# Performance work log

Measured on AMD Instinct MI355X. Metric: run time of the kernel, lower is better.

## Reference

```python
import jax, jax.numpy as jnp
import numpy as np

B, S, D, H, HD, F = 8, 1024, 512, 8, 64, 2048
EPS = 1e-6

def rmsnorm(x, w):
    var = jnp.mean(x * x, axis=-1, keepdims=True)
    return w * (x * jax.lax.rsqrt(var + EPS))

def setup_inputs() -> dict:
    key = jax.random.key(0)
    ks = jax.random.split(key, 10)
    sd = 512 ** -0.5
    return {
        "primals_1": jax.random.normal(ks[0], (D, D), jnp.float32) * sd,
        "primals_2": jax.random.normal(ks[1], (D, D), jnp.float32) * sd,
        "primals_3": jax.random.normal(ks[2], (D, D), jnp.float32) * sd,
        "primals_4": jax.random.normal(ks[3], (D, D), jnp.float32) * sd,
        "primals_5": jax.random.uniform(ks[4], (D,), jnp.float32, 0.5, 1.5),
        "primals_6": jax.random.normal(ks[5], (F, D), jnp.float32) * sd,
        "primals_7": jax.random.normal(ks[6], (D, F), jnp.float32) * (F ** -0.5),
        "primals_8": jax.random.uniform(ks[7], (D,), jnp.float32, 0.5, 1.5),
        "primals_9": jax.random.normal(ks[8], (B, S, D), jnp.float32),
        "primals_10": jax.random.normal(ks[9], (B, H, S, S), jnp.float32) * 0.1,
    }

def reference(primals_1, primals_2, primals_3, primals_4, primals_5,
              primals_6, primals_7, primals_8, primals_9, primals_10):
    x = primals_9
    # --- self-attention sublayer ---
    h = rmsnorm(x, primals_5)                      # [B,S,D]
    # T5: no 1/sqrt(head_dim) scaling
    q = (h @ primals_3.T).reshape(B, S, H, HD).transpose(0, 2, 1, 3)  # [B,H,S,HD]
    k = (h @ primals_1.T).reshape(B, S, H, HD).transpose(0, 2, 1, 3)
    v = (h @ primals_4.T).reshape(B, S, H, HD).transpose(0, 2, 1, 3)
    scores = jnp.einsum('bhqd,bhkd->bhqk', q, k) + primals_10        # [B,H,S,S]
    attn = jax.nn.softmax(scores, axis=-1)
    ctx = jnp.einsum('bhqk,bhkd->bhqd', attn, v)                     # [B,H,S,HD]
    ctx = ctx.transpose(0, 2, 1, 3).reshape(B, S, D)
    x = x + ctx @ primals_2.T                       # residual add_1
    # --- FFN sublayer ---
    h2 = rmsnorm(x, primals_8)
    ff = jax.nn.relu(h2 @ primals_6.T)              # [B,S,F]
    out = x + ff @ primals_7.T                      # add_3
    return out
```

## Files before the change

kernel.cpp:

```cpp
#include <hip/hip_runtime.h>

#define B_ 8
#define S_ 1024
#define D_ 512
#define H_ 8
#define HD_ 64
#define F_ 2048

typedef unsigned short u16;
typedef unsigned int u32;
typedef __attribute__((ext_vector_type(8))) short bf16x8;
typedef __attribute__((ext_vector_type(4))) float f32x4;

__device__ __forceinline__ float bf2f(u16 u) {
  union { unsigned int i; float f; } v; v.i = ((unsigned int)u) << 16; return v.f;
}
__device__ __forceinline__ u16 f2bf(float f) {
  union { float f; unsigned int i; } v; v.f = f;
  unsigned int r = v.i + 0x7fffu + ((v.i >> 16) & 1u);
  return (u16)(r >> 16);
}

__device__ __forceinline__ void gl2lds16(const u16* g, u16* lds) {
  __builtin_amdgcn_global_load_lds(
      (const __attribute__((address_space(1))) unsigned int*)g,
      (__attribute__((address_space(3))) unsigned int*)lds, 16, 0, 0);
}

__global__ __launch_bounds__(256) void cvt_w_k(const float* __restrict__ wq, const float* __restrict__ wk,
                                               const float* __restrict__ wv, const float* __restrict__ wo,
                                               const float* __restrict__ wf1, const float* __restrict__ wf2,
                                               u16* __restrict__ dst) {
  size_t gid = (size_t)blockIdx.x * 256 + threadIdx.x;
  size_t e0 = gid * 4;
  const float* src; size_t loc;
  if      (e0 <  262144) { src = wq;  loc = e0; }
  else if (e0 <  524288) { src = wk;  loc = e0 -  262144; }
  else if (e0 <  786432) { src = wv;  loc = e0 -  524288; }
  else if (e0 < 1048576) { src = wo;  loc = e0 -  786432; }
  else if (e0 < 2097152) { src = wf1; loc = e0 - 1048576; }
  else                   { src = wf2; loc = e0 - 2097152; }
  float4 v = *(const float4*)(src + loc);
  ushort4 o; o.x = f2bf(v.x); o.y = f2bf(v.y); o.z = f2bf(v.z); o.w = f2bf(v.w);
  *(ushort4*)(dst + e0) = o;
}

template <int IN_BF16>
__global__ __launch_bounds__(256) void rmsnorm_k(const void* __restrict__ xv,
                                                 const float* __restrict__ w,
                                                 u16* __restrict__ out) {
  int row = blockIdx.x;
  int tid = threadIdx.x;
  float x0, x1;
  if (IN_BF16) {
    u32 v = ((const u32*)((const u16*)xv + (size_t)row * D_))[tid];
    x0 = bf2f((u16)(v & 0xffffu)); x1 = bf2f((u16)(v >> 16));
  } else {
    float2 v = ((const float2*)((const float*)xv + (size_t)row * D_))[tid];
    x0 = v.x; x1 = v.y;
  }
  float s = x0 * x0 + x1 * x1;
#pragma unroll
  for (int off = 32; off >= 1; off >>= 1) s += __shfl_xor(s, off, 64);
  __shared__ float red[4];
  int lane = tid & 63, wid = tid >> 6;
  if (lane == 0) red[wid] = s;
  __syncthreads();
  float tot = red[0] + red[1] + red[2] + red[3];
  float inv = rsqrtf(tot * (1.0f / D_) + 1e-6f);
  float2 wv = ((const float2*)w)[tid];
  u32 o = (u32)f2bf(x0 * inv * wv.x) | ((u32)f2bf(x1 * inv * wv.y) << 16);
  ((u32*)(out + (size_t)row * D_))[tid] = o;
}

template <int RELU, int RMODE, int OF32, int BM>
__global__ __launch_bounds__(256) void gemm_mfma_k(const u16* __restrict__ A,
                                                   const u16* __restrict__ W,
                                                   const void* __restrict__ Rv,
                                                   void* __restrict__ Cv,
                                                   int M, int N, int K) {
  constexpr int MI  = BM / 32;
  constexpr int ACH = BM / 16;
  __shared__ __align__(16) u16 As[BM * 32];
  __shared__ __align__(16) u16 Bs[128 * 32];
  int tid = threadIdx.x;
  int w = tid >> 6, l = tid & 63;
  int quad = l >> 4, l16 = l & 15;
  int m0 = blockIdx.y * BM, n0 = blockIdx.x * 128;
  int wr = (w >> 1) * (BM / 2), wc = (w & 1) * 64;

  int c_sw = (l & 3) ^ ((l >> 2) & 3);
  int r_in = l >> 2;
  int swz = quad ^ (l16 & 3);

  f32x4 acc[MI][4];
#pragma unroll
  for (int i = 0; i < MI; i++)
#pragma unroll
    for (int j = 0; j < 4; j++) acc[i][j] = (f32x4)(0.0f);

  for (int k0 = 0; k0 < K; k0 += 32) {
    __syncthreads();
#pragma unroll
    for (int t = 0; t < (ACH + 8) / 4; t++) {
      int ch = w * ((ACH + 8) / 4) + t;
      const u16* src; u16* dst;
      if (ch < ACH) { src = A + (size_t)(m0 + ch * 16 + r_in) * K;        dst = As + ch * 512; }
      else          { src = W + (size_t)(n0 + (ch - ACH) * 16 + r_in) * K; dst = Bs + (ch - ACH) * 512; }
      gl2lds16(src + k0 + c_sw * 8, dst);
    }
    __syncthreads();
    bf16x8 af[MI], bf[4];
#pragma unroll
    for (int i = 0; i < MI; i++)
      af[i] = *(const bf16x8*)(As + (wr + i * 16 + l16) * 32 + swz * 8);
#pragma unroll
    for (int j = 0; j < 4; j++)
      bf[j] = *(const bf16x8*)(Bs + (wc + j * 16 + l16) * 32 + swz * 8);
#pragma unroll
    for (int i = 0; i < MI; i++)
#pragma unroll
      for (int j = 0; j < 4; j++)
        acc[i][j] = __builtin_amdgcn_mfma_f32_16x16x32_bf16(af[i], bf[j], acc[i][j], 0, 0, 0);
  }

#pragma unroll
  for (int i = 0; i < MI; i++)
#pragma unroll
    for (int r = 0; r < 4; r++) {
      int mrow = m0 + wr + i * 16 + quad * 4 + r;
      size_t base = (size_t)mrow * N + n0 + wc + l16;
#pragma unroll
      for (int j = 0; j < 4; j++) {
        float v = acc[i][j][r];
        if (RELU) v = fmaxf(v, 0.0f);
        if (RMODE == 1) v += ((const float*)Rv)[base + j * 16];
        if (RMODE == 2) v += bf2f(((const u16*)Rv)[base + j * 16]);
        if (OF32) ((float*)Cv)[base + j * 16] = v;
        else      ((u16*)Cv)[base + j * 16]   = f2bf(v);
      }
    }
}

__global__ __launch_bounds__(256) void transpose_v_k(const u16* __restrict__ qkv,
                                                     u16* __restrict__ vt) {
  __shared__ u16 T[64][72];
  int t = threadIdx.x;
  int s0 = blockIdx.x * 64, h = blockIdx.y, b = blockIdx.z;
  int skey = t >> 3, dch = (t & 7) * 8;
  int rot = dch >> 3;
#pragma unroll
  for (int rnd = 0; rnd < 2; rnd++) {
    int s = s0 + skey + rnd * 32;
    bf16x8 vv = *(const bf16x8*)(qkv + ((size_t)(b * S_) + s) * 1536 + 1024 + h * HD_ + dch);
#pragma unroll
    for (int i = 0; i < 8; i++) {
      int ii = (i + rot) & 7;
      T[dch + ii][skey + rnd * 32] = (u16)((short*)&vv)[ii];
    }
  }
  __syncthreads();
  int d = t >> 2, kc = (t & 3) * 16;
  bf16x8 a0 = *(const bf16x8*)(&T[d][kc]);
  bf16x8 a1 = *(const bf16x8*)(&T[d][kc + 8]);
  u16* dst = vt + ((size_t)(b * H_ + h) * HD_ + d) * S_ + s0 + kc;
  *(bf16x8*)dst       = a0;
  *(bf16x8*)(dst + 8) = a1;
}

__global__ __launch_bounds__(256) void attn_v3_k(const u16* __restrict__ qkv,
                                                 const u16* __restrict__ vt,
                                                 const float* __restrict__ bias,
                                                 u16* __restrict__ ctx) {
  int tid = threadIdx.x;
  int w = tid >> 6, lane = tid & 63;
  int quad = lane >> 4, l16 = lane & 15;
  int h = blockIdx.y, b = blockIdx.z;
  int q0 = blockIdx.x * 64;

  __shared__ __align__(16) u16 Pl[4][16 * 72];

  const u16* qrow = qkv + ((size_t)(b * S_) + q0 + w * 16 + l16) * 1536 + h * HD_;
  bf16x8 qf0 = *(const bf16x8*)(qrow + quad * 8);
  bf16x8 qf1 = *(const bf16x8*)(qrow + 32 + quad * 8);

  float mr[4], lr[4];
  f32x4 Oacc[4];
#pragma unroll
  for (int r = 0; r < 4; r++) { mr[r] = -1e30f; lr[r] = 0.0f; }
#pragma unroll
  for (int nt = 0; nt < 4; nt++) Oacc[nt] = (f32x4)(0.0f);

  const float* bpw = bias + ((size_t)((b * H_ + h) * S_) + q0 + w * 16) * S_;
  const u16* kbase = qkv + (size_t)(b * S_) * 1536 + 512 + h * HD_ + quad * 8;
  const u16* vbase = vt + (size_t)((b * H_ + h) * HD_) * S_ + quad * 8;

  for (int kt = 0; kt < S_; kt += 64) {
    f32x4 sg[4];
    __builtin_amdgcn_s_setprio(1);
#pragma unroll
    for (int g = 0; g < 4; g++) {
      const u16* kp = kbase + (size_t)(kt + g * 16 + l16) * 1536;
      bf16x8 kf0 = *(const bf16x8*)kp;
      bf16x8 kf1 = *(const bf16x8*)(kp + 32);
      f32x4 a = (f32x4)(0.0f);
      a = __builtin_amdgcn_mfma_f32_16x16x32_bf16(qf0, kf0, a, 0, 0, 0);
      a = __builtin_amdgcn_mfma_f32_16x16x32_bf16(qf1, kf1, a, 0, 0, 0);
      sg[g] = a;
    }
    __builtin_amdgcn_s_setprio(0);
#pragma unroll
    for (int r = 0; r < 4; r++) {
      size_t bro = (size_t)(quad * 4 + r) * S_ + kt + l16;
      float b0 = bpw[bro];
      float b1 = bpw[bro + 16];
      float b2 = bpw[bro + 32];
      float b3 = bpw[bro + 48];
      float s0 = sg[0][r] + b0, s1 = sg[1][r] + b1, s2 = sg[2][r] + b2, s3 = sg[3][r] + b3;
      float t = fmaxf(fmaxf(s0, s1), fmaxf(s2, s3));
      t = fmaxf(t, __shfl_xor(t, 1, 64));
      t = fmaxf(t, __shfl_xor(t, 2, 64));
      t = fmaxf(t, __shfl_xor(t, 4, 64));
      t = fmaxf(t, __shfl_xor(t, 8, 64));
      float mn = fmaxf(mr[r], t);
      float alpha = __expf(mr[r] - mn);
      float p0 = __expf(s0 - mn), p1 = __expf(s1 - mn);
      float p2 = __expf(s2 - mn), p3 = __expf(s3 - mn);
      float rs = (p0 + p1) + (p2 + p3);
      rs += __shfl_xor(rs, 1, 64);
      rs += __shfl_xor(rs, 2, 64);
      rs += __shfl_xor(rs, 4, 64);
      rs += __shfl_xor(rs, 8, 64);
      lr[r] = lr[r] * alpha + rs;
      mr[r] = mn;
#pragma unroll
      for (int nt = 0; nt < 4; nt++) Oacc[nt][r] *= alpha;
      u16* prow = &Pl[w][(quad * 4 + r) * 72];
      prow[l16]      = f2bf(p0);
      prow[16 + l16] = f2bf(p1);
      prow[32 + l16] = f2bf(p2);
      prow[48 + l16] = f2bf(p3);
    }
    bf16x8 pf0 = *(const bf16x8*)(&Pl[w][l16 * 72 + quad * 8]);
    bf16x8 pf1 = *(const bf16x8*)(&Pl[w][l16 * 72 + 32 + quad * 8]);
    __builtin_amdgcn_s_setprio(1);
#pragma unroll
    for (int nt = 0; nt < 4; nt++) {
      const u16* vp = vbase + (size_t)(nt * 16 + l16) * S_ + kt;
      bf16x8 vf0 = *(const bf16x8*)vp;
      bf16x8 vf1 = *(const bf16x8*)(vp + 32);
      Oacc[nt] = __builtin_amdgcn_mfma_f32_16x16x32_bf16(pf0, vf0, Oacc[nt], 0, 0, 0);
      Oacc[nt] = __builtin_amdgcn_mfma_f32_16x16x32_bf16(pf1, vf1, Oacc[nt], 0, 0, 0);
    }
    __builtin_amdgcn_s_setprio(0);
  }

  size_t obase = ((size_t)(b * S_) + q0 + w * 16) * D_ + h * HD_;
#pragma unroll
  for (int r = 0; r < 4; r++) {
    float inv = 1.0f / lr[r];
    int qr = quad * 4 + r;
#pragma unroll
    for (int nt = 0; nt < 4; nt++) {
      ctx[obase + (size_t)qr * D_ + nt * 16 + l16] = f2bf(Oacc[nt][r] * inv);
    }
  }
}

extern "C" void kernel_launch(void* const* d_in, const int* in_sizes, int n_in,
                              void* d_out, int out_size, void* d_ws, size_t ws_size,
                              hipStream_t stream) {
  const float* Wk   = (const float*)d_in[0];
  const float* Wo   = (const float*)d_in[1];
  const float* Wq   = (const float*)d_in[2];
  const float* Wv   = (const float*)d_in[3];
  const float* g1   = (const float*)d_in[4];
  const float* Wf1  = (const float*)d_in[5];
  const float* Wf2  = (const float*)d_in[6];
  const float* g2   = (const float*)d_in[7];
  const float* X    = (const float*)d_in[8];
  const float* bias = (const float*)d_in[9];
  float* out = (float*)d_out;

  const size_t MD = (size_t)B_ * S_ * D_;
  u16* wbf   = (u16*)d_ws;
  u16* Wqkvb = wbf;
  u16* Wob   = wbf +  786432;
  u16* Wf1b  = wbf + 1048576;
  u16* Wf2b  = wbf + 2097152;
  u16* h     = wbf + 3145728;
  u16* qkv   = h + MD;
  u16* vtb   = qkv + 3 * MD;
  u16* ctx   = vtb + MD;
  u16* ff    = ctx + MD;
  u16* x1    = qkv;
  u16* h2    = h;

  dim3 blk(256);
  const int M = B_ * S_;

  cvt_w_k<<<3072, blk, 0, stream>>>(Wq, Wk, Wv, Wo, Wf1, Wf2, wbf);

  rmsnorm_k<0><<<M, blk, 0, stream>>>(X, g1, h);

  dim3 gqkv(1536 / 128, M / 128);
  gemm_mfma_k<0, 0, 0, 128><<<gqkv, blk, 0, stream>>>(h, Wqkvb, nullptr, qkv, M, 1536, D_);

  dim3 gt(S_ / 64, H_, B_);
  transpose_v_k<<<gt, blk, 0, stream>>>(qkv, vtb);

  dim3 ga(S_ / 64, H_, B_);
  attn_v3_k<<<ga, blk, 0, stream>>>(qkv, vtb, bias, ctx);

  dim3 g512b(D_ / 128, M / 64);
  gemm_mfma_k<0, 1, 0, 64><<<g512b, blk, 0, stream>>>(ctx, Wob, X, x1, M, D_, D_);

  rmsnorm_k<1><<<M, blk, 0, stream>>>(x1, g2, h2);

  dim3 gff1(F_ / 128, M / 128);
  gemm_mfma_k<1, 0, 0, 128><<<gff1, blk, 0, stream>>>(h2, Wf1b, nullptr, ff, M, F_, D_);

  gemm_mfma_k<0, 2, 1, 64><<<g512b, blk, 0, stream>>>(ff, Wf2b, x1, out, M, D_, F_);
}
```

Measured before the change: 644.9 us.

## Stage K/V tiles in LDS with double buffering and prefetch bias in attention

```diff
diff --git a/kernel.cpp b/kernel.cpp
--- a/kernel.cpp
+++ b/kernel.cpp
@@ -168,17 +168,43 @@
   *(bf16x8*)(dst + 8) = a1;
 }
 
-__global__ __launch_bounds__(256) void attn_v3_k(const u16* __restrict__ qkv,
-                                                 const u16* __restrict__ vt,
-                                                 const float* __restrict__ bias,
-                                                 u16* __restrict__ ctx) {
+
+__device__ __forceinline__ void attn_stage(const u16* __restrict__ qkv,
+                                           const u16* __restrict__ vt,
+                                           u16* kvbuf, int b, int h, int kt,
+                                           int w, int lane) {
+#pragma unroll
+  for (int i = 0; i < 2; i++) {
+    int slot = w * 2 + i;
+    int bufid = slot >> 2;
+    int qq = slot & 3;
+    int srow = qq * 16 + (lane >> 2);
+    int slc = (lane & 3) ^ (srow & 3);
+    const u16* src;
+    if (bufid == 0)
+      src = qkv + ((size_t)(b * S_) + kt + srow) * 1536 + 512 + h * HD_ + slc * 8;
+    else if (bufid == 1)
+      src = qkv + ((size_t)(b * S_) + kt + srow) * 1536 + 544 + h * HD_ + slc * 8;
+    else if (bufid == 2)
+      src = vt + ((size_t)((b * H_ + h) * HD_) + srow) * S_ + kt + slc * 8;
+    else
+      src = vt + ((size_t)((b * H_ + h) * HD_) + srow) * S_ + kt + 32 + slc * 8;
+    gl2lds16(src, kvbuf + bufid * 2048 + qq * 512);
+  }
+}
+
+__global__ __launch_bounds__(512, 4) void attn_v4_k(const u16* __restrict__ qkv,
+                                                    const u16* __restrict__ vt,
+                                                    const float* __restrict__ bias,
+                                                    u16* __restrict__ ctx) {
   int tid = threadIdx.x;
   int w = tid >> 6, lane = tid & 63;
   int quad = lane >> 4, l16 = lane & 15;
   int h = blockIdx.y, b = blockIdx.z;
-  int q0 = blockIdx.x * 64;
-
-  __shared__ __align__(16) u16 Pl[4][16 * 72];
+  int q0 = blockIdx.x * 128;
+
+  __shared__ __align__(16) u16 KV[2][4 * 2048];
+  __shared__ __align__(16) u16 Pl[8][16 * 72];
 
   const u16* qrow = qkv + ((size_t)(b * S_) + q0 + w * 16 + l16) * 1536 + h * HD_;
   bf16x8 qf0 = *(const bf16x8*)(qrow + quad * 8);
@@ -192,37 +218,57 @@
   for (int nt = 0; nt < 4; nt++) Oacc[nt] = (f32x4)(0.0f);
 
   const float* bpw = bias + ((size_t)((b * H_ + h) * S_) + q0 + w * 16) * S_;
-  const u16* kbase = qkv + (size_t)(b * S_) * 1536 + 512 + h * HD_ + quad * 8;
-  const u16* vbase = vt + (size_t)((b * H_ + h) * HD_) * S_ + quad * 8;
-
-  for (int kt = 0; kt < S_; kt += 64) {
+
+  float bc[4][4], bn[4][4];
+#pragma unroll
+  for (int r = 0; r < 4; r++) {
+    size_t bro = (size_t)(quad * 4 + r) * S_ + l16;
+    bc[r][0] = bpw[bro];      bc[r][1] = bpw[bro + 16];
+    bc[r][2] = bpw[bro + 32]; bc[r][3] = bpw[bro + 48];
+  }
+
+  int cur = 0;
+  attn_stage(qkv, vt, &KV[0][0], b, h, 0, w, lane);
+
+  for (int t = 0; t < 16; t++) {
+    int kt = t * 64;
+    __syncthreads();
+    if (t < 15) {
+      attn_stage(qkv, vt, &KV[cur ^ 1][0], b, h, kt + 64, w, lane);
+#pragma unroll
+      for (int r = 0; r < 4; r++) {
+        size_t bro = (size_t)(quad * 4 + r) * S_ + kt + 64 + l16;
+        bn[r][0] = bpw[bro];      bn[r][1] = bpw[bro + 16];
+        bn[r][2] = bpw[bro + 32]; bn[r][3] = bpw[bro + 48];
+      }
+    }
+    const u16* kvb = &KV[cur][0];
+
     f32x4 sg[4];
     __builtin_amdgcn_s_setprio(1);
 #pragma unroll
     for (int g = 0; g < 4; g++) {
-      const u16* kp = kbase + (size_t)(kt + g * 16 + l16) * 1536;
-      bf16x8 kf0 = *(const bf16x8*)kp;
-      bf16x8 kf1 = *(const bf16x8*)(kp + 32);
+      int row = g * 16 + l16;
+      int sw = quad ^ (row & 3);
+      bf16x8 kf0 = *(const bf16x8*)(kvb + row * 32 + sw * 8);
+      bf16x8 kf1 = *(const bf16x8*)(kvb + 2048 + row * 32 + sw * 8);
       f32x4 a = (f32x4)(0.0f);
       a = __builtin_amdgcn_mfma_f32_16x16x32_bf16(qf0, kf0, a, 0, 0, 0);
       a = __builtin_amdgcn_mfma_f32_16x16x32_bf16(qf1, kf1, a, 0, 0, 0);
       sg[g] = a;
     }
     __builtin_amdgcn_s_setprio(0);
+
 #pragma unroll
     for (int r = 0; r < 4; r++) {
-      size_t bro = (size_t)(quad * 4 + r) * S_ + kt + l16;
-      float b0 = bpw[bro];
-      float b1 = bpw[bro + 16];
-      float b2 = bpw[bro + 32];
-      float b3 = bpw[bro + 48];
-      float s0 = sg[0][r] + b0, s1 = sg[1][r] + b1, s2 = sg[2][r] + b2, s3 = sg[3][r] + b3;
-      float t = fmaxf(fmaxf(s0, s1), fmaxf(s2, s3));
-      t = fmaxf(t, __shfl_xor(t, 1, 64));
-      t = fmaxf(t, __shfl_xor(t, 2, 64));
-      t = fmaxf(t, __shfl_xor(t, 4, 64));
-      t = fmaxf(t, __shfl_xor(t, 8, 64));
-      float mn = fmaxf(mr[r], t);
+      float s0 = sg[0][r] + bc[r][0], s1 = sg[1][r] + bc[r][1];
+      float s2 = sg[2][r] + bc[r][2], s3 = sg[3][r] + bc[r][3];
+      float t4 = fmaxf(fmaxf(s0, s1), fmaxf(s2, s3));
+      t4 = fmaxf(t4, __shfl_xor(t4, 1, 64));
+      t4 = fmaxf(t4, __shfl_xor(t4, 2, 64));
+      t4 = fmaxf(t4, __shfl_xor(t4, 4, 64));
+      t4 = fmaxf(t4, __shfl_xor(t4, 8, 64));
+      float mn = fmaxf(mr[r], t4);
       float alpha = __expf(mr[r] - mn);
       float p0 = __expf(s0 - mn), p1 = __expf(s1 - mn);
       float p2 = __expf(s2 - mn), p3 = __expf(s3 - mn);
@@ -243,16 +289,26 @@
     }
     bf16x8 pf0 = *(const bf16x8*)(&Pl[w][l16 * 72 + quad * 8]);
     bf16x8 pf1 = *(const bf16x8*)(&Pl[w][l16 * 72 + 32 + quad * 8]);
+
     __builtin_amdgcn_s_setprio(1);
 #pragma unroll
     for (int nt = 0; nt < 4; nt++) {
-      const u16* vp = vbase + (size_t)(nt * 16 + l16) * S_ + kt;
-      bf16x8 vf0 = *(const bf16x8*)vp;
-      bf16x8 vf1 = *(const bf16x8*)(vp + 32);
+      int row = nt * 16 + l16;
+      int sw = quad ^ (row & 3);
+      bf16x8 vf0 = *(const bf16x8*)(kvb + 4096 + row * 32 + sw * 8);
+      bf16x8 vf1 = *(const bf16x8*)(kvb + 6144 + row * 32 + sw * 8);
       Oacc[nt] = __builtin_amdgcn_mfma_f32_16x16x32_bf16(pf0, vf0, Oacc[nt], 0, 0, 0);
       Oacc[nt] = __builtin_amdgcn_mfma_f32_16x16x32_bf16(pf1, vf1, Oacc[nt], 0, 0, 0);
     }
     __builtin_amdgcn_s_setprio(0);
+
+    if (t < 15) {
+#pragma unroll
+      for (int r = 0; r < 4; r++)
+#pragma unroll
+        for (int j = 0; j < 4; j++) bc[r][j] = bn[r][j];
+    }
+    cur ^= 1;
   }
 
   size_t obase = ((size_t)(b * S_) + q0 + w * 16) * D_ + h * HD_;
@@ -309,16 +365,16 @@
   dim3 gt(S_ / 64, H_, B_);
   transpose_v_k<<<gt, blk, 0, stream>>>(qkv, vtb);
 
-  dim3 ga(S_ / 64, H_, B_);
-  attn_v3_k<<<ga, blk, 0, stream>>>(qkv, vtb, bias, ctx);
-
-  dim3 g512b(D_ / 128, M / 64);
-  gemm_mfma_k<0, 1, 0, 64><<<g512b, blk, 0, stream>>>(ctx, Wob, X, x1, M, D_, D_);
+  dim3 ga(S_ / 128, H_, B_);
+  attn_v4_k<<<ga, dim3(512), 0, stream>>>(qkv, vtb, bias, ctx);
+
+  dim3 g512(D_ / 128, M / 128);
+  gemm_mfma_k<0, 1, 0, 128><<<g512, blk, 0, stream>>>(ctx, Wob, X, x1, M, D_, D_);
 
   rmsnorm_k<1><<<M, blk, 0, stream>>>(x1, g2, h2);
 
   dim3 gff1(F_ / 128, M / 128);
   gemm_mfma_k<1, 0, 0, 128><<<gff1, blk, 0, stream>>>(h2, Wf1b, nullptr, ff, M, F_, D_);
 
-  gemm_mfma_k<0, 2, 1, 64><<<g512b, blk, 0, stream>>>(ff, Wf2b, x1, out, M, D_, F_);
-}
+  gemm_mfma_k<0, 2, 1, 128><<<g512, blk, 0, stream>>>(ff, Wf2b, x1, out, M, D_, F_);
+}
```

Result: faster. 577.4 us (-10.5%).
